# Kernel tuning notes

Hardware: AMD Instinct MI355X
Metric: run time of the kernel (lower is better)

Reference implementation:

```python
import jax, jax.numpy as jnp
import numpy as np

B, N, D, R, H = 8192, 256, 6, 3, 32


def setup_inputs() -> dict:
    key = jax.random.key(0)
    ks = jax.random.split(key, 8)
    neighbor_states = jax.random.normal(ks[0], (B, N, D), dtype=jnp.float32)
    neighbor_roles = jax.random.randint(ks[1], (B, N), 0, R, dtype=jnp.int32)
    neighbor_mask = jax.random.randint(ks[2], (B, N), 0, 2, dtype=jnp.int32).astype(jnp.bool_)
    trust_weights = jax.random.uniform(ks[3], (B, N), dtype=jnp.float32)
    # per-role MLP params: Linear(D,H) -> ReLU -> Linear(H,1)
    s1 = 1.0 / np.sqrt(D)
    s2 = 1.0 / np.sqrt(H)
    W1 = jax.random.uniform(ks[4], (R, D, H), minval=-s1, maxval=s1, dtype=jnp.float32)
    b1 = jax.random.uniform(ks[5], (R, H), minval=-s1, maxval=s1, dtype=jnp.float32)
    W2 = jax.random.uniform(ks[6], (R, H), minval=-s2, maxval=s2, dtype=jnp.float32)
    b2 = jax.random.uniform(ks[7], (R,), minval=-s2, maxval=s2, dtype=jnp.float32)
    return {
        "neighbor_states": neighbor_states,
        "neighbor_roles": neighbor_roles,
        "neighbor_mask": neighbor_mask,
        "trust_weights": trust_weights,
        "W1": W1, "b1": b1, "W2": W2, "b2": b2,
    }


def reference(neighbor_states, neighbor_roles, neighbor_mask, trust_weights, W1, b1, W2, b2):
    maskf = neighbor_mask.astype(jnp.float32)          # [B, N]
    tw = trust_weights * maskf                          # [B, N]
    # per-role attention scores, vectorized over roles: [B, R, N]
    h = jax.nn.relu(jnp.einsum('bnd,rdh->brnh', neighbor_states, W1) + b1[None, :, None, :])
    scores = jnp.einsum('brnh,rh->brn', h, W2) + b2[None, :, None]
    role_mask = (neighbor_roles[:, None, :] == jnp.arange(R)[None, :, None]).astype(jnp.float32) * maskf[:, None, :]
    scores = scores * role_mask                         # NOTE: multiplicative masking, as in original
    m = scores.max(axis=2, keepdims=True)
    e = jnp.exp(scores - m) * role_mask
    aw = e / (e.sum(axis=2, keepdims=True) + 1e-8)      # [B, R, N]
    w = aw * tw[:, None, :]
    ws = jnp.clip(w.sum(axis=2, keepdims=True), 1e-8)   # [B, R, 1]
    mf = jnp.einsum('brn,bnd->brd', w, neighbor_states) / ws  # [B, R, D]
    return mf.reshape(mf.shape[0], R * D)               # concat roles along last dim
```

## Files before the change

### kernel.cpp

```cpp
#include <hip/hip_runtime.h>
#include <math.h>

#define NBATCH 8192
#define NNEI 256
#define NROLE 3
#define NHID 32
#define NDIM 6
#define SSTRIDE 12

typedef float v2f __attribute__((ext_vector_type(2)));
typedef unsigned long long ull;

__device__ __forceinline__ void barrier_lds_only() {
  __asm__ __volatile__("" ::: "memory");
  __builtin_amdgcn_s_waitcnt(0xC07F);
  __builtin_amdgcn_s_barrier();
  __asm__ __volatile__("" ::: "memory");
}

template <int CTRL>
__device__ __forceinline__ float dppmov(float x) {
  return __int_as_float(__builtin_amdgcn_update_dpp(
      0, __float_as_int(x), CTRL, 0xF, 0xF, true));
}

__device__ __forceinline__ float wavesum_dpp(float v) {
  v += dppmov<0x111>(v);
  v += dppmov<0x112>(v);
  v += dppmov<0x114>(v);
  v += dppmov<0x118>(v);
  v += dppmov<0x142>(v);
  v += dppmov<0x143>(v);
  return v;
}
__device__ __forceinline__ float total63(float v) {
  return __int_as_float(
      __builtin_amdgcn_readlane(__float_as_int(wavesum_dpp(v)), 63));
}

__device__ __forceinline__ float mlp_score(const float x0, const float x1,
                                           const float x2, const float x3,
                                           const float x4, const float x5,
                                           const float* __restrict__ w1,
                                           const float* __restrict__ bb,
                                           const float* __restrict__ w2,
                                           const float b2v) {
  const float x[NDIM] = {x0, x1, x2, x3, x4, x5};
  v2f ac0 = {0.f, 0.f}, ac1 = {0.f, 0.f}, ac2 = {0.f, 0.f}, ac3 = {0.f, 0.f};
#pragma unroll
  for (int h = 0; h < NHID; h += 8) {
    v2f a0 = *(const v2f*)(bb + h + 0);
    v2f a1 = *(const v2f*)(bb + h + 2);
    v2f a2 = *(const v2f*)(bb + h + 4);
    v2f a3 = *(const v2f*)(bb + h + 6);
#pragma unroll
    for (int d = 0; d < NDIM; ++d) {
      const float xv = x[d];
      const v2f xv2 = {xv, xv};
      const float* wc = w1 + d * NHID + h;
      a0 += xv2 * (*(const v2f*)(wc + 0));
      a1 += xv2 * (*(const v2f*)(wc + 2));
      a2 += xv2 * (*(const v2f*)(wc + 4));
      a3 += xv2 * (*(const v2f*)(wc + 6));
    }
    a0.x = fmaxf(a0.x, 0.f); a0.y = fmaxf(a0.y, 0.f);
    a1.x = fmaxf(a1.x, 0.f); a1.y = fmaxf(a1.y, 0.f);
    a2.x = fmaxf(a2.x, 0.f); a2.y = fmaxf(a2.y, 0.f);
    a3.x = fmaxf(a3.x, 0.f); a3.y = fmaxf(a3.y, 0.f);
    ac0 += a0 * (*(const v2f*)(w2 + h + 0));
    ac1 += a1 * (*(const v2f*)(w2 + h + 2));
    ac2 += a2 * (*(const v2f*)(w2 + h + 4));
    ac3 += a3 * (*(const v2f*)(w2 + h + 6));
  }
  const v2f st = (ac0 + ac1) + (ac2 + ac3);
  return b2v + st.x + st.y;
}

__global__ __launch_bounds__(192) void hmf_main(
    const float* __restrict__ states,
    const int* __restrict__ roles,
    const int* __restrict__ maskp,
    const float* __restrict__ trust,
    const float* __restrict__ W1,
    const float* __restrict__ b1,
    const float* __restrict__ W2,
    const float* __restrict__ b2g,
    float* __restrict__ out) {
  const int b = blockIdx.x;
  const int tid = threadIdx.x;
  const int wave = tid >> 6;
  const int lane = tid & 63;

  __shared__ float ssort[NNEI * SSTRIDE];
  __shared__ alignas(16) int scnt4[4];

  const size_t rowb = (size_t)b * NNEI;

  const size_t idxA = rowb + (size_t)(wave * 64 + lane);
  const int roleA = roles[idxA];
  const int maskA = maskp[idxA];
  const float twA = trust[idxA];
  const float* spA = states + idxA * (size_t)NDIM;
  const float2 aA = *(const float2*)(spA);
  const float2 aB = *(const float2*)(spA + 2);
  const float2 aC = *(const float2*)(spA + 4);

  const bool have2 = (wave == 0);
  int roleB = 0, maskB = 0;
  float twB = 0.f;
  float2 bA = {0.f, 0.f}, bB = {0.f, 0.f}, bC = {0.f, 0.f};
  if (have2) {
    const size_t idxB = rowb + (size_t)(192 + lane);
    roleB = roles[idxB];
    maskB = maskp[idxB];
    twB = trust[idxB];
    const float* spB = states + idxB * (size_t)NDIM;
    bA = *(const float2*)(spB);
    bB = *(const float2*)(spB + 2);
    bC = *(const float2*)(spB + 4);
  }

  {
    const bool active = (maskA != 0);
    const ull bal0 = __ballot(active && (roleA == 0));
    const ull bal1 = __ballot(active && (roleA == 1));
    const ull bal2 = __ballot(active && (roleA == 2));
    const int c0 = __popcll(bal0);
    const int c1 = __popcll(bal1);
    const int c2 = __popcll(bal2);
    if (lane == 0) scnt4[wave] = c0 | (c1 << 8) | (c2 << 16);
    if (active) {
      const ull mybal = (roleA == 0) ? bal0 : (roleA == 1) ? bal1 : bal2;
      const int rank = __popcll(mybal & ((1ull << lane) - 1ull));
      const int pre = ((roleA >= 1) ? c0 : 0) + ((roleA >= 2) ? c1 : 0);
      const int pos = wave * 64 + pre + rank;
      float* dst = ssort + pos * SSTRIDE;
      *(float4*)dst = make_float4(aA.x, aA.y, aB.x, aB.y);
      *(float4*)(dst + 4) = make_float4(aC.x, aC.y, twA, 0.f);
    }
  }
  if (have2) {
    const bool active = (maskB != 0);
    const ull bal0 = __ballot(active && (roleB == 0));
    const ull bal1 = __ballot(active && (roleB == 1));
    const ull bal2 = __ballot(active && (roleB == 2));
    const int c0 = __popcll(bal0);
    const int c1 = __popcll(bal1);
    const int c2 = __popcll(bal2);
    if (lane == 0) scnt4[3] = c0 | (c1 << 8) | (c2 << 16);
    if (active) {
      const ull mybal = (roleB == 0) ? bal0 : (roleB == 1) ? bal1 : bal2;
      const int rank = __popcll(mybal & ((1ull << lane) - 1ull));
      const int pre = ((roleB >= 1) ? c0 : 0) + ((roleB >= 2) ? c1 : 0);
      const int pos = 192 + pre + rank;
      float* dst = ssort + pos * SSTRIDE;
      *(float4*)dst = make_float4(bA.x, bA.y, bB.x, bB.y);
      *(float4*)(dst + 4) = make_float4(bC.x, bC.y, twB, 0.f);
    }
  }
  barrier_lds_only();

  {
    const int r = __builtin_amdgcn_readfirstlane(wave);
    const int4 scv = *(const int4*)scnt4;
    int cwv[4], prw[4];
#pragma unroll
    for (int w = 0; w < 4; ++w) {
      const int pk = __builtin_amdgcn_readfirstlane((&scv.x)[w]);
      const int a0 = pk & 0xFF;
      const int a1 = (pk >> 8) & 0xFF;
      const int a2 = (pk >> 16) & 0xFF;
      cwv[w] = (r == 0) ? a0 : (r == 1) ? a1 : a2;
      prw[w] = ((r >= 1) ? a0 : 0) + ((r >= 2) ? a1 : 0);
    }
    const int acc0 = cwv[0];
    const int acc1 = acc0 + cwv[1];
    const int acc2 = acc1 + cwv[2];
    const int cnt = acc2 + cwv[3];

    const float* w1 = W1 + r * (NDIM * NHID);
    const float* bb = b1 + r * NHID;
    const float* w2 = W2 + r * NHID;
    const float b2v = b2g[r];

    float q0, q1, q2, q3, q4, q5, q6, q7;

    if (cnt <= 64) {
      const bool act = lane < cnt;
      const bool s1 = lane >= acc0;
      const bool s2 = lane >= acc1;
      const bool s3 = lane >= acc2;
      int sub = s1 ? acc0 : 0; sub = s2 ? acc1 : sub; sub = s3 ? acc2 : sub;
      int wb = s1 ? 64 : 0;    wb = s2 ? 128 : wb;    wb = s3 ? 192 : wb;
      int pr = s1 ? prw[1] : prw[0]; pr = s2 ? prw[2] : pr; pr = s3 ? prw[3] : pr;
      int pos = wb + pr + (lane - sub);
      pos = (pos > NNEI - 1) ? (NNEI - 1) : pos;
      const float* s = ssort + pos * SSTRIDE;
      float4 v4 = *(const float4*)s;
      float4 vb = *(const float4*)(s + 4);
      float tw = vb.z;
      if (!act) {
        v4 = make_float4(0.f, 0.f, 0.f, 0.f);
        vb = make_float4(0.f, 0.f, 0.f, 0.f);
        tw = 0.f;
      }
      const float sc = mlp_score(v4.x, v4.y, v4.z, v4.w, vb.x, vb.y, w1, bb, w2, b2v);
      const float e = act ? __expf(sc) : 0.f;
      const float et = e * tw;
      q0 = e; q1 = et;
      q2 = et * v4.x; q3 = et * v4.y; q4 = et * v4.z;
      q5 = et * v4.w; q6 = et * vb.x; q7 = et * vb.y;
    } else {
      q0 = q1 = q2 = q3 = q4 = q5 = q6 = q7 = 0.f;
      const int nch = (cnt + 63) >> 6;
      for (int c = 0; c < nch; ++c) {
        const int jj = c * 64 + lane;
        const bool act = jj < cnt;
        const bool s1 = jj >= acc0;
        const bool s2 = jj >= acc1;
        const bool s3 = jj >= acc2;
        int sub = s1 ? acc0 : 0; sub = s2 ? acc1 : sub; sub = s3 ? acc2 : sub;
        int wb = s1 ? 64 : 0;    wb = s2 ? 128 : wb;    wb = s3 ? 192 : wb;
        int pr = s1 ? prw[1] : prw[0]; pr = s2 ? prw[2] : pr; pr = s3 ? prw[3] : pr;
        int pos = wb + pr + (jj - sub);
        pos = (pos > NNEI - 1) ? (NNEI - 1) : pos;
        pos = (pos < 0) ? 0 : pos;
        const float* s = ssort + pos * SSTRIDE;
        float4 v4 = *(const float4*)s;
        float4 vb = *(const float4*)(s + 4);
        float tw = vb.z;
        if (!act) {
          v4 = make_float4(0.f, 0.f, 0.f, 0.f);
          vb = make_float4(0.f, 0.f, 0.f, 0.f);
          tw = 0.f;
        }
        const float sc = mlp_score(v4.x, v4.y, v4.z, v4.w, vb.x, vb.y, w1, bb, w2, b2v);
        const float e = act ? __expf(sc) : 0.f;
        const float et = e * tw;
        q0 += e; q1 += et;
        q2 = fmaf(et, v4.x, q2); q3 = fmaf(et, v4.y, q3);
        q4 = fmaf(et, v4.z, q4); q5 = fmaf(et, v4.w, q5);
        q6 = fmaf(et, vb.x, q6); q7 = fmaf(et, vb.y, q7);
      }
    }

    const float Se  = total63(q0);
    const float Set = total63(q1);
    const float T2  = total63(q2);
    const float T3  = total63(q3);
    const float T4  = total63(q4);
    const float T5  = total63(q5);
    const float T6  = total63(q6);
    const float T7  = total63(q7);

    const float denom = Se + 1e-8f;
    const float ws = fmaxf(Set / denom, 1e-8f);
    const float scale = 1.0f / (denom * ws);
    if (lane >= 2 && lane < 8) {
      float num = T2;
      num = (lane == 3) ? T3 : num;
      num = (lane == 4) ? T4 : num;
      num = (lane == 5) ? T5 : num;
      num = (lane == 6) ? T6 : num;
      num = (lane == 7) ? T7 : num;
      out[(size_t)b * (NROLE * NDIM) + r * NDIM + (lane - 2)] = num * scale;
    }
  }
}

extern "C" void kernel_launch(void* const* d_in, const int* in_sizes, int n_in,
                              void* d_out, int out_size, void* d_ws, size_t ws_size,
                              hipStream_t stream) {
  const float* states = (const float*)d_in[0];
  const int* roles = (const int*)d_in[1];
  const int* maskp = (const int*)d_in[2];
  const float* trust = (const float*)d_in[3];
  const float* W1 = (const float*)d_in[4];
  const float* b1 = (const float*)d_in[5];
  const float* W2 = (const float*)d_in[6];
  const float* b2 = (const float*)d_in[7];
  float* out = (float*)d_out;

  hmf_main<<<NBATCH, 192, 0, stream>>>(states, roles, maskp, trust, W1, b1, W2, b2, out);
}
```

Baseline: 118.2 us.

## Make blocks persistent over four batches and prefetch the next batch's registers

The grid shrinks from one block per batch to 2048 blocks, each looping over four batches strided by the grid size. The next batch's roles, mask, trust and states are loaded into registers while the current batch is scattered and scored. This aims to hide global-load latency behind compute and to amortise block launch and weight-pointer setup. In exchange it raises register pressure, adds a second barrier per iteration, and leaves fewer blocks to fill the GPU.

```diff
diff --git a/kernel.cpp b/kernel.cpp
--- a/kernel.cpp
+++ b/kernel.cpp
@@ -6,6 +6,8 @@
 #define NROLE 3
 #define NHID 32
 #define NDIM 6
+#define NWG 2048
+#define NBPB 4
 #define SSTRIDE 12
 
 typedef float v2f __attribute__((ext_vector_type(2)));
@@ -76,6 +78,64 @@
   return b2v + st.x + st.y;
 }
 
+struct BR {
+  int rlA, mkA; float twA; float2 aA, aB, aC;
+  int rlB, mkB; float twB; float2 bA, bB, bC;
+};
+
+__device__ __forceinline__ void load_batch(const float* __restrict__ states,
+                                           const int* __restrict__ roles,
+                                           const int* __restrict__ maskp,
+                                           const float* __restrict__ trust,
+                                           const int b, const int wave,
+                                           const int lane, const bool have2,
+                                           BR& r) {
+  const size_t rowb = (size_t)b * NNEI;
+  const size_t idxA = rowb + (size_t)(wave * 64 + lane);
+  r.rlA = roles[idxA];
+  r.mkA = maskp[idxA];
+  r.twA = trust[idxA];
+  const float* spA = states + idxA * (size_t)NDIM;
+  r.aA = *(const float2*)(spA);
+  r.aB = *(const float2*)(spA + 2);
+  r.aC = *(const float2*)(spA + 4);
+  if (have2) {
+    const size_t idxB = rowb + (size_t)(192 + lane);
+    r.rlB = roles[idxB];
+    r.mkB = maskp[idxB];
+    r.twB = trust[idxB];
+    const float* spB = states + idxB * (size_t)NDIM;
+    r.bA = *(const float2*)(spB);
+    r.bB = *(const float2*)(spB + 2);
+    r.bC = *(const float2*)(spB + 4);
+  }
+}
+
+__device__ __forceinline__ void scatter_one(float* __restrict__ ssort,
+                                            int* __restrict__ scnt4,
+                                            const int chunk, const int lane,
+                                            const int rl, const int mk,
+                                            const float tw, const float2 a,
+                                            const float2 bq, const float2 c) {
+  const bool active = (mk != 0);
+  const ull bal0 = __ballot(active && (rl == 0));
+  const ull bal1 = __ballot(active && (rl == 1));
+  const ull bal2 = __ballot(active && (rl == 2));
+  const int c0 = __popcll(bal0);
+  const int c1 = __popcll(bal1);
+  const int c2 = __popcll(bal2);
+  if (lane == 0) scnt4[chunk] = c0 | (c1 << 8) | (c2 << 16);
+  if (active) {
+    const ull mybal = (rl == 0) ? bal0 : (rl == 1) ? bal1 : bal2;
+    const int rank = __popcll(mybal & ((1ull << lane) - 1ull));
+    const int pre = ((rl >= 1) ? c0 : 0) + ((rl >= 2) ? c1 : 0);
+    const int pos = chunk * 64 + pre + rank;
+    float* dst = ssort + pos * SSTRIDE;
+    *(float4*)dst = make_float4(a.x, a.y, bq.x, bq.y);
+    *(float4*)(dst + 4) = make_float4(c.x, c.y, tw, 0.f);
+  }
+}
+
 __global__ __launch_bounds__(192) void hmf_main(
     const float* __restrict__ states,
     const int* __restrict__ roles,
@@ -86,145 +146,67 @@
     const float* __restrict__ W2,
     const float* __restrict__ b2g,
     float* __restrict__ out) {
-  const int b = blockIdx.x;
   const int tid = threadIdx.x;
   const int wave = tid >> 6;
   const int lane = tid & 63;
+  const bool have2 = (wave == 0);
 
   __shared__ float ssort[NNEI * SSTRIDE];
   __shared__ alignas(16) int scnt4[4];
 
-  const size_t rowb = (size_t)b * NNEI;
-
-  const size_t idxA = rowb + (size_t)(wave * 64 + lane);
-  const int roleA = roles[idxA];
-  const int maskA = maskp[idxA];
-  const float twA = trust[idxA];
-  const float* spA = states + idxA * (size_t)NDIM;
-  const float2 aA = *(const float2*)(spA);
-  const float2 aB = *(const float2*)(spA + 2);
-  const float2 aC = *(const float2*)(spA + 4);
-
-  const bool have2 = (wave == 0);
-  int roleB = 0, maskB = 0;
-  float twB = 0.f;
-  float2 bA = {0.f, 0.f}, bB = {0.f, 0.f}, bC = {0.f, 0.f};
-  if (have2) {
-    const size_t idxB = rowb + (size_t)(192 + lane);
-    roleB = roles[idxB];
-    maskB = maskp[idxB];
-    twB = trust[idxB];
-    const float* spB = states + idxB * (size_t)NDIM;
-    bA = *(const float2*)(spB);
-    bB = *(const float2*)(spB + 2);
-    bC = *(const float2*)(spB + 4);
-  }
-
-  {
-    const bool active = (maskA != 0);
-    const ull bal0 = __ballot(active && (roleA == 0));
-    const ull bal1 = __ballot(active && (roleA == 1));
-    const ull bal2 = __ballot(active && (roleA == 2));
-    const int c0 = __popcll(bal0);
-    const int c1 = __popcll(bal1);
-    const int c2 = __popcll(bal2);
-    if (lane == 0) scnt4[wave] = c0 | (c1 << 8) | (c2 << 16);
-    if (active) {
-      const ull mybal = (roleA == 0) ? bal0 : (roleA == 1) ? bal1 : bal2;
-      const int rank = __popcll(mybal & ((1ull << lane) - 1ull));
-      const int pre = ((roleA >= 1) ? c0 : 0) + ((roleA >= 2) ? c1 : 0);
-      const int pos = wave * 64 + pre + rank;
-      float* dst = ssort + pos * SSTRIDE;
-      *(float4*)dst = make_float4(aA.x, aA.y, aB.x, aB.y);
-      *(float4*)(dst + 4) = make_float4(aC.x, aC.y, twA, 0.f);
-    }
-  }
-  if (have2) {
-    const bool active = (maskB != 0);
-    const ull bal0 = __ballot(active && (roleB == 0));
-    const ull bal1 = __ballot(active && (roleB == 1));
-    const ull bal2 = __ballot(active && (roleB == 2));
-    const int c0 = __popcll(bal0);
-    const int c1 = __popcll(bal1);
-    const int c2 = __popcll(bal2);
-    if (lane == 0) scnt4[3] = c0 | (c1 << 8) | (c2 << 16);
-    if (active) {
-      const ull mybal = (roleB == 0) ? bal0 : (roleB == 1) ? bal1 : bal2;
-      const int rank = __popcll(mybal & ((1ull << lane) - 1ull));
-      const int pre = ((roleB >= 1) ? c0 : 0) + ((roleB >= 2) ? c1 : 0);
-      const int pos = 192 + pre + rank;
-      float* dst = ssort + pos * SSTRIDE;
-      *(float4*)dst = make_float4(bA.x, bA.y, bB.x, bB.y);
-      *(float4*)(dst + 4) = make_float4(bC.x, bC.y, twB, 0.f);
-    }
-  }
-  barrier_lds_only();
-
-  {
-    const int r = __builtin_amdgcn_readfirstlane(wave);
-    const int4 scv = *(const int4*)scnt4;
-    int cwv[4], prw[4];
+  const int r = __builtin_amdgcn_readfirstlane(wave);
+  const float* w1 = W1 + r * (NDIM * NHID);
+  const float* bb = b1 + r * NHID;
+  const float* w2 = W2 + r * NHID;
+  const float b2v = b2g[r];
+
+  BR cur, nxt;
+  load_batch(states, roles, maskp, trust, blockIdx.x, wave, lane, have2, cur);
+
 #pragma unroll
-    for (int w = 0; w < 4; ++w) {
-      const int pk = __builtin_amdgcn_readfirstlane((&scv.x)[w]);
-      const int a0 = pk & 0xFF;
-      const int a1 = (pk >> 8) & 0xFF;
-      const int a2 = (pk >> 16) & 0xFF;
-      cwv[w] = (r == 0) ? a0 : (r == 1) ? a1 : a2;
-      prw[w] = ((r >= 1) ? a0 : 0) + ((r >= 2) ? a1 : 0);
-    }
-    const int acc0 = cwv[0];
-    const int acc1 = acc0 + cwv[1];
-    const int acc2 = acc1 + cwv[2];
-    const int cnt = acc2 + cwv[3];
-
-    const float* w1 = W1 + r * (NDIM * NHID);
-    const float* bb = b1 + r * NHID;
-    const float* w2 = W2 + r * NHID;
-    const float b2v = b2g[r];
-
-    float q0, q1, q2, q3, q4, q5, q6, q7;
-
-    if (cnt <= 64) {
-      const bool act = lane < cnt;
-      const bool s1 = lane >= acc0;
-      const bool s2 = lane >= acc1;
-      const bool s3 = lane >= acc2;
-      int sub = s1 ? acc0 : 0; sub = s2 ? acc1 : sub; sub = s3 ? acc2 : sub;
-      int wb = s1 ? 64 : 0;    wb = s2 ? 128 : wb;    wb = s3 ? 192 : wb;
-      int pr = s1 ? prw[1] : prw[0]; pr = s2 ? prw[2] : pr; pr = s3 ? prw[3] : pr;
-      int pos = wb + pr + (lane - sub);
-      pos = (pos > NNEI - 1) ? (NNEI - 1) : pos;
-      const float* s = ssort + pos * SSTRIDE;
-      float4 v4 = *(const float4*)s;
-      float4 vb = *(const float4*)(s + 4);
-      float tw = vb.z;
-      if (!act) {
-        v4 = make_float4(0.f, 0.f, 0.f, 0.f);
-        vb = make_float4(0.f, 0.f, 0.f, 0.f);
-        tw = 0.f;
+  for (int t = 0; t < NBPB; ++t) {
+    if (t + 1 < NBPB) {
+      load_batch(states, roles, maskp, trust, blockIdx.x + (t + 1) * NWG,
+                 wave, lane, have2, nxt);
+    }
+
+    scatter_one(ssort, scnt4, wave, lane, cur.rlA, cur.mkA, cur.twA,
+                cur.aA, cur.aB, cur.aC);
+    if (have2) {
+      scatter_one(ssort, scnt4, 3, lane, cur.rlB, cur.mkB, cur.twB,
+                  cur.bA, cur.bB, cur.bC);
+    }
+    barrier_lds_only();
+
+    {
+      const int4 scv = *(const int4*)scnt4;
+      int cwv[4], prw[4];
+#pragma unroll
+      for (int w = 0; w < 4; ++w) {
+        const int pk = __builtin_amdgcn_readfirstlane((&scv.x)[w]);
+        const int a0 = pk & 0xFF;
+        const int a1 = (pk >> 8) & 0xFF;
+        const int a2 = (pk >> 16) & 0xFF;
+        cwv[w] = (r == 0) ? a0 : (r == 1) ? a1 : a2;
+        prw[w] = ((r >= 1) ? a0 : 0) + ((r >= 2) ? a1 : 0);
       }
-      const float sc = mlp_score(v4.x, v4.y, v4.z, v4.w, vb.x, vb.y, w1, bb, w2, b2v);
-      const float e = act ? __expf(sc) : 0.f;
-      const float et = e * tw;
-      q0 = e; q1 = et;
-      q2 = et * v4.x; q3 = et * v4.y; q4 = et * v4.z;
-      q5 = et * v4.w; q6 = et * vb.x; q7 = et * vb.y;
-    } else {
-      q0 = q1 = q2 = q3 = q4 = q5 = q6 = q7 = 0.f;
-      const int nch = (cnt + 63) >> 6;
-      for (int c = 0; c < nch; ++c) {
-        const int jj = c * 64 + lane;
-        const bool act = jj < cnt;
-        const bool s1 = jj >= acc0;
-        const bool s2 = jj >= acc1;
-        const bool s3 = jj >= acc2;
+      const int acc0 = cwv[0];
+      const int acc1 = acc0 + cwv[1];
+      const int acc2 = acc1 + cwv[2];
+      const int cnt = acc2 + cwv[3];
+
+      float q0, q1, q2, q3, q4, q5, q6, q7;
+
+      if (cnt <= 64) {
+        const bool act = lane < cnt;
+        const bool s1 = lane >= acc0;
+        const bool s2 = lane >= acc1;
+        const bool s3 = lane >= acc2;
         int sub = s1 ? acc0 : 0; sub = s2 ? acc1 : sub; sub = s3 ? acc2 : sub;
         int wb = s1 ? 64 : 0;    wb = s2 ? 128 : wb;    wb = s3 ? 192 : wb;
         int pr = s1 ? prw[1] : prw[0]; pr = s2 ? prw[2] : pr; pr = s3 ? prw[3] : pr;
-        int pos = wb + pr + (jj - sub);
+        int pos = wb + pr + (lane - sub);
         pos = (pos > NNEI - 1) ? (NNEI - 1) : pos;
-        pos = (pos < 0) ? 0 : pos;
         const float* s = ssort + pos * SSTRIDE;
         float4 v4 = *(const float4*)s;
         float4 vb = *(const float4*)(s + 4);
@@ -237,33 +219,70 @@
         const float sc = mlp_score(v4.x, v4.y, v4.z, v4.w, vb.x, vb.y, w1, bb, w2, b2v);
         const float e = act ? __expf(sc) : 0.f;
         const float et = e * tw;
-        q0 += e; q1 += et;
-        q2 = fmaf(et, v4.x, q2); q3 = fmaf(et, v4.y, q3);
-        q4 = fmaf(et, v4.z, q4); q5 = fmaf(et, v4.w, q5);
-        q6 = fmaf(et, vb.x, q6); q7 = fmaf(et, vb.y, q7);
+        q0 = e; q1 = et;
+        q2 = et * v4.x; q3 = et * v4.y; q4 = et * v4.z;
+        q5 = et * v4.w; q6 = et * vb.x; q7 = et * vb.y;
+      } else {
+        q0 = q1 = q2 = q3 = q4 = q5 = q6 = q7 = 0.f;
+        const int nch = (cnt + 63) >> 6;
+        for (int c = 0; c < nch; ++c) {
+          const int jj = c * 64 + lane;
+          const bool act = jj < cnt;
+          const bool s1 = jj >= acc0;
+          const bool s2 = jj >= acc1;
+          const bool s3 = jj >= acc2;
+          int sub = s1 ? acc0 : 0; sub = s2 ? acc1 : sub; sub = s3 ? acc2 : sub;
+          int wb = s1 ? 64 : 0;    wb = s2 ? 128 : wb;    wb = s3 ? 192 : wb;
+          int pr = s1 ? prw[1] : prw[0]; pr = s2 ? prw[2] : pr; pr = s3 ? prw[3] : pr;
+          int pos = wb + pr + (jj - sub);
+          pos = (pos > NNEI - 1) ? (NNEI - 1) : pos;
+          pos = (pos < 0) ? 0 : pos;
+          const float* s = ssort + pos * SSTRIDE;
+          float4 v4 = *(const float4*)s;
+          float4 vb = *(const float4*)(s + 4);
+          float tw = vb.z;
+          if (!act) {
+            v4 = make_float4(0.f, 0.f, 0.f, 0.f);
+            vb = make_float4(0.f, 0.f, 0.f, 0.f);
+            tw = 0.f;
+          }
+          const float sc = mlp_score(v4.x, v4.y, v4.z, v4.w, vb.x, vb.y, w1, bb, w2, b2v);
+          const float e = act ? __expf(sc) : 0.f;
+          const float et = e * tw;
+          q0 += e; q1 += et;
+          q2 = fmaf(et, v4.x, q2); q3 = fmaf(et, v4.y, q3);
+          q4 = fmaf(et, v4.z, q4); q5 = fmaf(et, v4.w, q5);
+          q6 = fmaf(et, vb.x, q6); q7 = fmaf(et, vb.y, q7);
+        }
       }
-    }
-
-    const float Se  = total63(q0);
-    const float Set = total63(q1);
-    const float T2  = total63(q2);
-    const float T3  = total63(q3);
-    const float T4  = total63(q4);
-    const float T5  = total63(q5);
-    const float T6  = total63(q6);
-    const float T7  = total63(q7);
-
-    const float denom = Se + 1e-8f;
-    const float ws = fmaxf(Set / denom, 1e-8f);
-    const float scale = 1.0f / (denom * ws);
-    if (lane >= 2 && lane < 8) {
-      float num = T2;
-      num = (lane == 3) ? T3 : num;
-      num = (lane == 4) ? T4 : num;
-      num = (lane == 5) ? T5 : num;
-      num = (lane == 6) ? T6 : num;
-      num = (lane == 7) ? T7 : num;
-      out[(size_t)b * (NROLE * NDIM) + r * NDIM + (lane - 2)] = num * scale;
+
+      const float Se  = total63(q0);
+      const float Set = total63(q1);
+      const float T2  = total63(q2);
+      const float T3  = total63(q3);
+      const float T4  = total63(q4);
+      const float T5  = total63(q5);
+      const float T6  = total63(q6);
+      const float T7  = total63(q7);
+
+      const float denom = Se + 1e-8f;
+      const float ws = fmaxf(Set / denom, 1e-8f);
+      const float scale = 1.0f / (denom * ws);
+      if (lane >= 2 && lane < 8) {
+        float num = T2;
+        num = (lane == 3) ? T3 : num;
+        num = (lane == 4) ? T4 : num;
+        num = (lane == 5) ? T5 : num;
+        num = (lane == 6) ? T6 : num;
+        num = (lane == 7) ? T7 : num;
+        out[(size_t)(blockIdx.x + t * NWG) * (NROLE * NDIM) + r * NDIM +
+            (lane - 2)] = num * scale;
+      }
+    }
+
+    if (t + 1 < NBPB) {
+      barrier_lds_only();
+      cur = nxt;
     }
   }
 }
@@ -281,5 +300,5 @@
   const float* b2 = (const float*)d_in[7];
   float* out = (float*)d_out;
 
-  hmf_main<<<NBATCH, 192, 0, stream>>>(states, roles, maskp, trust, W1, b1, W2, b2, out);
-}
+  hmf_main<<<NWG, 192, 0, stream>>>(states, roles, maskp, trust, W1, b1, W2, b2, out);
+}
```

Result: slower. 124.4 us (+5.2%).
